# Kernel tuning notes

Measured on AMD Instinct MI355X. Metric: run time of the kernel, lower is better.

The kernel has to match this reference:

```python
import jax, jax.numpy as jnp
import numpy as np

B, S, V, E, H, EMB = 512, 400, 50000, 512, 256, 128


def setup_inputs() -> dict:
    key = jax.random.key(0)
    ks = jax.random.split(key, 20)
    f = lambda i, shape, s=1.0: jax.random.normal(ks[i], shape, jnp.float32) * s
    return dict(
        coverage=jax.random.uniform(ks[0], (B, S), jnp.float32),
        enc_out=f(1, (B, S, E)),
        h0=f(2, (B, H)),
        c0=f(3, (B, H)),
        attn=jax.nn.softmax(f(4, (B, S)), axis=1),
        dec_input=jax.random.randint(ks[5], (B, 1), 0, V),
        enc_inputs=jax.random.randint(ks[6], (B, S), 0, V),
        emb_table=f(7, (V, EMB), 0.02),
        W_ih=f(8, (4 * H, EMB + E), 0.05),
        W_hh=f(9, (4 * H, H), 0.05),
        b_ih=jnp.zeros(4 * H, jnp.float32),
        b_hh=jnp.zeros(4 * H, jnp.float32),
        awh_W=f(10, (H, E), 0.05),
        awh_b=jnp.zeros(H, jnp.float32),
        aws_W=f(11, (H, H), 0.05),
        aws_b=jnp.zeros(H, jnp.float32),
        awc=jax.random.uniform(ks[12], (H,), jnp.float32),
        av=jax.random.uniform(ks[13], (H,), jnp.float32),
        wh=jax.random.uniform(ks[14], (E,), jnp.float32),
        ws=jax.random.uniform(ks[15], (H,), jnp.float32),
        wx=jax.random.uniform(ks[16], (EMB,), jnp.float32),
        v_W=f(17, (V, H), 0.05),
        v_b=jnp.zeros(V, jnp.float32),
    )


def reference(coverage, enc_out, h0, c0, attn, dec_input, enc_inputs,
              emb_table, W_ih, W_hh, b_ih, b_hh,
              awh_W, awh_b, aws_W, aws_b, awc, av,
              wh, ws, wx, v_W, v_b):
    b, s, e = enc_out.shape
    vocab = emb_table.shape[0]

    # context = bmm(attn[B,1,S], enc_out[B,S,E]) -> [B,1,E]
    context = jnp.einsum('bs,bse->be', attn, enc_out)  # [B,E]
    embed = emb_table[dec_input[:, 0]]                 # [B,EMB]
    x = jnp.concatenate([context, embed], axis=1)      # [B,E+EMB]

    # LSTMCell (torch gate order: i, f, g, o)
    gates = x @ W_ih.T + b_ih + h0 @ W_hh.T + b_hh     # [B,4H]
    i, f_, g, o = jnp.split(gates, 4, axis=1)
    c_t = jax.nn.sigmoid(f_) * c0 + jax.nn.sigmoid(i) * jnp.tanh(g)
    h_t = jax.nn.sigmoid(o) * jnp.tanh(c_t)

    p_vocab = jax.nn.softmax(h_t @ v_W.T + v_b, axis=1)  # [B,V]
    p_gen = jax.nn.sigmoid(context @ wh + h_t @ ws + embed @ wx)[:, None]  # [B,1]

    # Bahdanau attention with coverage
    wh_app = jnp.einsum('bse,he->bsh', enc_out, awh_W) + awh_b  # [B,S,H]
    ws_app = (h_t @ aws_W.T + aws_b)[:, None, :]                # [B,1,H]
    wc_app = coverage[:, :, None] * awc                         # [B,S,H]
    energy = jnp.tanh(wh_app + ws_app + wc_app) @ av            # [B,S]
    new_attn = jax.nn.softmax(energy, axis=1)

    coverage_loss = jnp.sum(jnp.minimum(new_attn, coverage))
    new_coverage = coverage + new_attn

    attn_scores = jnp.zeros((b, vocab), p_vocab.dtype).at[jnp.arange(b)[:, None], enc_inputs].set(new_attn)

    output = p_gen * p_vocab + (1.0 - p_gen) * attn_scores
    return output, new_coverage, (h_t, c_t), new_attn, coverage_loss
```

## Files before the change

### kernel.cpp

```cpp
#include <hip/hip_runtime.h>
#include <math.h>

#define Bd   512
#define Sd   400
#define Vd   50000
#define Ed   512
#define Hd   256
#define EMBd 128
#define XHs  896
#define Gd   1024

#define OFF_COV  25600000
#define OFF_H    25804800
#define OFF_C    25935872
#define OFF_ATTN 26066944
#define OFF_LOSS 26271744

#define WS_XH     0
#define WS_GATES  458752
#define WS_WSAPP  983040
#define WS_PGEN   1114112
#define WS_ENERGY 1114624
#define WS_LOSSB  1319424
#define WS_RMAX   1319936
#define WS_RSCALE 1320448
#define WS_HTBF   589824

typedef __attribute__((ext_vector_type(8))) short short8;
typedef __attribute__((ext_vector_type(4))) float f32x4;

__device__ __forceinline__ float sigmoid_f(float x){ return 1.f/(1.f + __expf(-x)); }
__device__ __forceinline__ float tanh_f(float x){ return 1.f - 2.f/(__expf(2.f*x) + 1.f); }

__device__ __forceinline__ void gload_lds16(const void* g, void* l){
  __builtin_amdgcn_global_load_lds((const __attribute__((address_space(1))) void*)g,
                                   (__attribute__((address_space(3))) void*)l, 16, 0, 0);
}

__global__ __launch_bounds__(256) void k_context(
    const float* __restrict__ attn, const float* __restrict__ enc_out,
    const float* __restrict__ h0, const int* __restrict__ dec_input,
    const float* __restrict__ emb_table, float* __restrict__ xh)
{
  int b = blockIdx.x, t = threadIdx.x;
  __shared__ float sa[Sd];
  for (int s = t; s < Sd; s += 256) sa[s] = attn[(size_t)b*Sd + s];
  __syncthreads();
  const float* ep = enc_out + (size_t)b*Sd*Ed;
  float acc0 = 0.f, acc1 = 0.f;
  #pragma unroll 4
  for (int s = 0; s < Sd; ++s){
    float a = sa[s];
    acc0 += a * ep[(size_t)s*Ed + t];
    acc1 += a * ep[(size_t)s*Ed + t + 256];
  }
  float* xrow = xh + (size_t)b*XHs;
  xrow[t]       = acc0;
  xrow[t + 256] = acc1;
  if (t < EMBd){
    int tok = dec_input[b];
    xrow[Ed + t] = emb_table[(size_t)tok*EMBd + t];
  }
  xrow[Ed + EMBd + t] = h0[(size_t)b*Hd + t];
}

__global__ __launch_bounds__(256) void k_gates(
    const float* __restrict__ xh, const float* __restrict__ W_ih,
    const float* __restrict__ W_hh, const float* __restrict__ b_ih,
    const float* __restrict__ b_hh, float* __restrict__ gates)
{
  __shared__ float Al[32*36];
  __shared__ float Wl[64*33];
  int tid = threadIdx.x;
  int col0 = blockIdx.x * 64;
  int row0 = blockIdx.y * 32;
  int cg = tid & 15, rg = tid >> 4;
  float acc[2][4] = {{0,0,0,0},{0,0,0,0}};
  int alr = tid >> 3, alk = (tid & 7) * 4;
  int wlj = tid >> 2, wlk = (tid & 3) * 8;
  for (int kt = 0; kt < 28; ++kt){
    int k0 = kt * 32;
    float4 a4 = *(const float4*)(xh + (size_t)(row0+alr)*XHs + k0 + alk);
    *(float4*)(Al + alr*36 + alk) = a4;
    {
      const float* src;
      if (k0 < Ed + EMBd) src = W_ih + (size_t)(col0+wlj)*(Ed+EMBd) + k0 + wlk;
      else                src = W_hh + (size_t)(col0+wlj)*Hd + (k0 - (Ed+EMBd)) + wlk;
      #pragma unroll
      for (int q = 0; q < 8; ++q) Wl[wlj*33 + wlk + q] = src[q];
    }
    __syncthreads();
    #pragma unroll 4
    for (int k = 0; k < 32; ++k){
      float a0 = Al[(rg*2+0)*36 + k];
      float a1 = Al[(rg*2+1)*36 + k];
      #pragma unroll
      for (int j = 0; j < 4; ++j){
        float w = Wl[(cg + 16*j)*33 + k];
        acc[0][j] += a0 * w;
        acc[1][j] += a1 * w;
      }
    }
    __syncthreads();
  }
  #pragma unroll
  for (int i = 0; i < 2; ++i){
    int row = row0 + rg*2 + i;
    #pragma unroll
    for (int j = 0; j < 4; ++j){
      int col = col0 + cg + 16*j;
      gates[(size_t)row*Gd + col] = acc[i][j] + b_ih[col] + b_hh[col];
    }
  }
}

__global__ __launch_bounds__(256) void k_lstm(
    const float* __restrict__ gates, const float* __restrict__ c0,
    float* __restrict__ dout)
{
  int idx = blockIdx.x*256 + threadIdx.x;
  int b = idx >> 8, h = idx & 255;
  const float* g = gates + (size_t)b*Gd;
  float xi = g[h], xf = g[Hd + h], xg = g[2*Hd + h], xo = g[3*Hd + h];
  float c  = sigmoid_f(xf)*c0[idx] + sigmoid_f(xi)*tanh_f(xg);
  float ht = sigmoid_f(xo)*tanh_f(c);
  dout[OFF_C + idx] = c;
  dout[OFF_H + idx] = ht;
}

__global__ __launch_bounds__(256) void k_wcvt(
    const float* __restrict__ W, short* __restrict__ hi, short* __restrict__ lo,
    const float* __restrict__ ht, short* __restrict__ htb)
{
  int bx = blockIdx.x;
  if (bx < 128){
    int i = bx*256 + threadIdx.x;
    float4 w = ((const float4*)W)[i];
    float xs[4] = {w.x, w.y, w.z, w.w};
    short h4[4], l4[4];
    #pragma unroll
    for (int j = 0; j < 4; ++j){
      unsigned u = __float_as_uint(xs[j]);
      h4[j] = (short)(u >> 16);
      float hf = __uint_as_float(u & 0xffff0000u);
      l4[j] = (short)(__float_as_uint(xs[j] - hf) >> 16);
    }
    ((short4*)hi)[i] = make_short4(h4[0], h4[1], h4[2], h4[3]);
    ((short4*)lo)[i] = make_short4(l4[0], l4[1], l4[2], l4[3]);
  } else {
    int i = (bx - 128)*256 + threadIdx.x;
    float4 w = ((const float4*)ht)[i];
    short h4[4];
    h4[0] = (short)((__float_as_uint(w.x) + 0x8000u) >> 16);
    h4[1] = (short)((__float_as_uint(w.y) + 0x8000u) >> 16);
    h4[2] = (short)((__float_as_uint(w.z) + 0x8000u) >> 16);
    h4[3] = (short)((__float_as_uint(w.w) + 0x8000u) >> 16);
    ((short4*)htb)[i] = make_short4(h4[0], h4[1], h4[2], h4[3]);
  }
}

__global__ __launch_bounds__(256) void k_post(
    const float* __restrict__ ht, const float* __restrict__ aws_W,
    const float* __restrict__ aws_b, const float* __restrict__ xh,
    const float* __restrict__ wh, const float* __restrict__ wsv,
    const float* __restrict__ wx, float* __restrict__ wsapp,
    float* __restrict__ pgen)
{
  int b = blockIdx.x, t = threadIdx.x;
  __shared__ float hrow[Hd];
  __shared__ float red[256];
  float htv = ht[(size_t)b*Hd + t];
  hrow[t] = htv;
  __syncthreads();
  const float4* w4 = (const float4*)(aws_W + (size_t)t*Hd);
  float acc = 0.f;
  #pragma unroll 4
  for (int k4 = 0; k4 < Hd/4; ++k4){
    float4 w = w4[k4];
    int k = k4*4;
    acc += hrow[k]*w.x + hrow[k+1]*w.y + hrow[k+2]*w.z + hrow[k+3]*w.w;
  }
  wsapp[(size_t)b*Hd + t] = acc + aws_b[t];
  const float* x = xh + (size_t)b*XHs;
  float part = x[t]*wh[t] + x[t+256]*wh[t+256];
  part += htv * wsv[t];
  if (t < EMBd) part += x[Ed + t] * wx[t];
  red[t] = part; __syncthreads();
  for (int off = 128; off > 0; off >>= 1){
    if (t < off) red[t] += red[t + off];
    __syncthreads();
  }
  if (t == 0) pgen[b] = sigmoid_f(red[0]);
}

__global__ __launch_bounds__(256) void k_energy_mfma(
    const float* __restrict__ enc_out, const short* __restrict__ Whi,
    const short* __restrict__ Wlo, const float* __restrict__ awh_b,
    const float* __restrict__ wsapp, const float* __restrict__ coverage,
    const float* __restrict__ awc, const float* __restrict__ av,
    float* __restrict__ energy)
{
  __shared__ short Ah[64*32], Alo[64*32];
  __shared__ short Bh[256*32], Blo[256*32];
  int tid = threadIdx.x;
  int wid = tid >> 6, lane = tid & 63;
  int row0 = blockIdx.x * 64;

  f32x4 acc[4][4] = {};

  int ar = tid >> 2, as_ = tid & 3;
  int a_st = ar*32 + (as_ ^ ((ar>>1)&3))*8;
  const float* ag = enc_out + (size_t)(row0 + ar)*Ed + as_*8;

  int b_r[4], b_s[4];
  #pragma unroll
  for (int c = 0; c < 4; ++c){
    int ch = wid*4 + c;
    int r  = ch*16 + (lane>>2);
    b_r[c] = r;
    b_s[c] = (lane&3) ^ ((r>>1)&3);
  }

  int n0 = wid*64;
  int a_rd[4], b_rd[4];
  #pragma unroll
  for (int m = 0; m < 4; ++m){
    int r = m*16 + (lane&15);
    a_rd[m] = r*32 + (((lane>>4) ^ ((r>>1)&3)))*8;
  }
  #pragma unroll
  for (int n = 0; n < 4; ++n){
    int c = n0 + n*16 + (lane&15);
    b_rd[n] = c*32 + (((lane>>4) ^ ((c>>1)&3)))*8;
  }

  for (int kt = 0; kt < Ed/32; ++kt){
    int k0 = kt*32;
    #pragma unroll
    for (int c = 0; c < 4; ++c){
      int ch = wid*4 + c;
      const short* gh = Whi + (size_t)b_r[c]*Ed + k0 + b_s[c]*8;
      const short* gl = Wlo + (size_t)b_r[c]*Ed + k0 + b_s[c]*8;
      gload_lds16(gh, &Bh[ch*512]);
      gload_lds16(gl, &Blo[ch*512]);
    }
    float4 a0 = *(const float4*)(ag + k0);
    float4 a1 = *(const float4*)(ag + k0 + 4);
    float xs[8] = {a0.x,a0.y,a0.z,a0.w,a1.x,a1.y,a1.z,a1.w};
    short8 h8, l8;
    #pragma unroll
    for (int q = 0; q < 8; ++q){
      unsigned u = __float_as_uint(xs[q]);
      h8[q] = (short)(u >> 16);
      float hf = __uint_as_float(u & 0xffff0000u);
      l8[q] = (short)(__float_as_uint(xs[q] - hf) >> 16);
    }
    *(short8*)&Ah[a_st]  = h8;
    *(short8*)&Alo[a_st] = l8;
    __syncthreads();

    short8 ah[4], al[4], bh[4], bl[4];
    #pragma unroll
    for (int m = 0; m < 4; ++m){
      ah[m] = *(const short8*)&Ah[a_rd[m]];
      al[m] = *(const short8*)&Alo[a_rd[m]];
    }
    #pragma unroll
    for (int n = 0; n < 4; ++n){
      bh[n] = *(const short8*)&Bh[b_rd[n]];
      bl[n] = *(const short8*)&Blo[b_rd[n]];
    }
    #pragma unroll
    for (int m = 0; m < 4; ++m){
      #pragma unroll
      for (int n = 0; n < 4; ++n){
        acc[m][n] = __builtin_amdgcn_mfma_f32_16x16x32_bf16(ah[m], bh[n], acc[m][n], 0, 0, 0);
        acc[m][n] = __builtin_amdgcn_mfma_f32_16x16x32_bf16(ah[m], bl[n], acc[m][n], 0, 0, 0);
        acc[m][n] = __builtin_amdgcn_mfma_f32_16x16x32_bf16(al[m], bh[n], acc[m][n], 0, 0, 0);
      }
    }
    __syncthreads();
  }

  float* red = (float*)Bh;
  int b0 = row0 / Sd;
  int b1 = b0 + 1; if (b1 > Bd-1) b1 = Bd-1;
  int split = (b0 + 1) * Sd;
  float avv[4], bbv[4], wcv[4], wv0[4], wv1[4];
  #pragma unroll
  for (int n = 0; n < 4; ++n){
    int h = n0 + n*16 + (lane&15);
    avv[n] = av[h]; bbv[n] = awh_b[h]; wcv[n] = awc[h];
    wv0[n] = wsapp[(size_t)b0*Hd + h];
    wv1[n] = wsapp[(size_t)b1*Hd + h];
  }
  #pragma unroll
  for (int m = 0; m < 4; ++m){
    #pragma unroll
    for (int j = 0; j < 4; ++j){
      int rt = m*16 + ((lane>>4)<<2) + j;
      int grow = row0 + rt;
      bool hib = (grow >= split);
      float cov = coverage[grow];
      float part = 0.f;
      #pragma unroll
      for (int n = 0; n < 4; ++n){
        float x = acc[m][n][j] + bbv[n] + (hib ? wv1[n] : wv0[n]) + cov*wcv[n];
        part += avv[n]*tanh_f(x);
      }
      part += __shfl_xor(part, 1, 16);
      part += __shfl_xor(part, 2, 16);
      part += __shfl_xor(part, 4, 16);
      part += __shfl_xor(part, 8, 16);
      if ((lane & 15) == 0) red[wid*64 + rt] = part;
    }
  }
  __syncthreads();
  if (tid < 64)
    energy[row0 + tid] = red[tid] + red[64 + tid] + red[128 + tid] + red[192 + tid];
}

__global__ __launch_bounds__(256) void k_attn_softmax(
    const float* __restrict__ energy, const float* __restrict__ coverage,
    float* __restrict__ dout, float* __restrict__ loss_b)
{
  int b = blockIdx.x, t = threadIdx.x;
  __shared__ float red[256];
  const float* e = energy + (size_t)b*Sd;
  float e0 = e[t];
  float e1 = (t + 256 < Sd) ? e[t+256] : -1e30f;
  red[t] = fmaxf(e0, e1); __syncthreads();
  for (int off = 128; off > 0; off >>= 1){
    if (t < off) red[t] = fmaxf(red[t], red[t+off]);
    __syncthreads();
  }
  float m = red[0]; __syncthreads();
  float p0 = __expf(e0 - m);
  float p1 = (t + 256 < Sd) ? __expf(e1 - m) : 0.f;
  red[t] = p0 + p1; __syncthreads();
  for (int off = 128; off > 0; off >>= 1){
    if (t < off) red[t] += red[t+off];
    __syncthreads();
  }
  float inv = 1.f / red[0]; __syncthreads();
  float* attn_o = dout + OFF_ATTN + (size_t)b*Sd;
  float* cov_o  = dout + OFF_COV  + (size_t)b*Sd;
  float a0 = p0 * inv;
  float cv0 = coverage[(size_t)b*Sd + t];
  attn_o[t] = a0; cov_o[t] = cv0 + a0;
  float lp = fminf(a0, cv0);
  if (t + 256 < Sd){
    float a1 = p1 * inv;
    float cv1 = coverage[(size_t)b*Sd + t + 256];
    attn_o[t+256] = a1; cov_o[t+256] = cv1 + a1;
    lp += fminf(a1, cv1);
  }
  red[t] = lp; __syncthreads();
  for (int off = 128; off > 0; off >>= 1){
    if (t < off) red[t] += red[t+off];
    __syncthreads();
  }
  if (t == 0) loss_b[b] = red[0];
}

__global__ void k_loss(const float* __restrict__ loss_b, float* __restrict__ dout)
{
  __shared__ float red[256];
  int t = threadIdx.x;
  red[t] = loss_b[t] + loss_b[t + 256];
  __syncthreads();
  for (int off = 128; off > 0; off >>= 1){
    if (t < off) red[t] += red[t+off];
    __syncthreads();
  }
  if (t == 0) dout[OFF_LOSS] = red[0];
}

__global__ __launch_bounds__(256) void k_logits_mfma(
    const short* __restrict__ ht_bf, const float* __restrict__ v_W,
    const float* __restrict__ v_b, float* __restrict__ out)
{
  __shared__ short Abf[128*32];
  __shared__ short Bbf[256*32];
  int tid = threadIdx.x;
  int wid = tid >> 6, lane = tid & 63;
  int col0 = blockIdx.x * 256;
  int row0 = blockIdx.y * 128;
  int wr0 = (wid & 1) * 64, wc0 = (wid >> 1) * 128;

  f32x4 acc[4][8] = {};

  int ac_r[2], ac_s[2];
  #pragma unroll
  for (int c = 0; c < 2; ++c){
    int ch = wid*2 + c;
    int r = ch*16 + (lane >> 2);
    ac_r[c] = r;
    ac_s[c] = (lane & 3) ^ ((r >> 1) & 3);
  }

  int vrow = col0 + tid; if (vrow > Vd - 1) vrow = Vd - 1;
  const float* bg = v_W + (size_t)vrow * Hd;
  int bsw = (tid >> 1) & 3;

  int a_rd[4], b_rd[8];
  #pragma unroll
  for (int m = 0; m < 4; ++m){
    int r = wr0 + m*16 + (lane & 15);
    a_rd[m] = r*32 + (((lane >> 4) ^ ((r >> 1) & 3)))*8;
  }
  #pragma unroll
  for (int n = 0; n < 8; ++n){
    int c = wc0 + n*16 + (lane & 15);
    b_rd[n] = c*32 + (((lane >> 4) ^ ((c >> 1) & 3)))*8;
  }

  for (int kt = 0; kt < Hd/32; ++kt){
    int k0 = kt * 32;
    #pragma unroll
    for (int c = 0; c < 2; ++c){
      const short* src = ht_bf + (size_t)(row0 + ac_r[c])*Hd + k0 + ac_s[c]*8;
      gload_lds16(src, &Abf[(wid*2 + c)*512]);
    }
    unsigned p[16];
    #pragma unroll
    for (int q = 0; q < 8; ++q){
      float4 f = *(const float4*)(bg + k0 + q*4);
      unsigned u0 = __float_as_uint(f.x) + 0x8000u;
      unsigned u1 = __float_as_uint(f.y) + 0x8000u;
      unsigned u2 = __float_as_uint(f.z) + 0x8000u;
      unsigned u3 = __float_as_uint(f.w) + 0x8000u;
      p[q*2]   = (u1 & 0xffff0000u) | (u0 >> 16);
      p[q*2+1] = (u3 & 0xffff0000u) | (u2 >> 16);
    }
    #pragma unroll
    for (int s = 0; s < 4; ++s){
      uint4 w4; w4.x = p[s*4]; w4.y = p[s*4+1]; w4.z = p[s*4+2]; w4.w = p[s*4+3];
      *(uint4*)&Bbf[tid*32 + (s ^ bsw)*8] = w4;
    }
    __syncthreads();
    short8 a[4];
    #pragma unroll
    for (int m = 0; m < 4; ++m) a[m] = *(const short8*)&Abf[a_rd[m]];
    #pragma unroll
    for (int n = 0; n < 8; ++n){
      short8 bfr = *(const short8*)&Bbf[b_rd[n]];
      #pragma unroll
      for (int m = 0; m < 4; ++m)
        acc[m][n] = __builtin_amdgcn_mfma_f32_16x16x32_bf16(a[m], bfr, acc[m][n], 0, 0, 0);
    }
    __syncthreads();
  }

  #pragma unroll
  for (int n = 0; n < 8; ++n){
    int col = col0 + wc0 + n*16 + (lane & 15);
    if (col < Vd){
      float bias = v_b[col];
      #pragma unroll
      for (int m = 0; m < 4; ++m){
        int rbase = row0 + wr0 + m*16 + ((lane >> 4) << 2);
        #pragma unroll
        for (int j = 0; j < 4; ++j)
          out[(size_t)(rbase + j)*Vd + col] = acc[m][n][j] + bias;
      }
    }
  }
}

__global__ __launch_bounds__(256) void k_vocab_stats(
    const float* __restrict__ logits, const float* __restrict__ pgen,
    float* __restrict__ rmax, float* __restrict__ rscale)
{
  int b = blockIdx.x, t = threadIdx.x;
  __shared__ float red[256];
  const float4* row = (const float4*)(logits + (size_t)b*Vd);
  float m = -1e30f;
  for (int i = t; i < Vd/4; i += 256){
    float4 x = row[i];
    m = fmaxf(m, fmaxf(fmaxf(x.x, x.y), fmaxf(x.z, x.w)));
  }
  red[t] = m; __syncthreads();
  for (int off = 128; off > 0; off >>= 1){
    if (t < off) red[t] = fmaxf(red[t], red[t+off]);
    __syncthreads();
  }
  m = red[0]; __syncthreads();
  float s = 0.f;
  for (int i = t; i < Vd/4; i += 256){
    float4 x = row[i];
    s += __expf(x.x-m) + __expf(x.y-m) + __expf(x.z-m) + __expf(x.w-m);
  }
  red[t] = s; __syncthreads();
  for (int off = 128; off > 0; off >>= 1){
    if (t < off) red[t] += red[t+off];
    __syncthreads();
  }
  if (t == 0){ rmax[b] = m; rscale[b] = pgen[b] / red[0]; }
}

__global__ __launch_bounds__(256) void k_vocab_norm(
    float* __restrict__ out, const float* __restrict__ rmax,
    const float* __restrict__ rscale)
{
  long long i4 = (long long)blockIdx.x*256 + threadIdx.x;
  int b = (int)(i4 / (Vd/4));
  float m = rmax[b], sc = rscale[b];
  float4* o = (float4*)out;
  float4 x = o[i4];
  x.x = sc*__expf(x.x - m); x.y = sc*__expf(x.y - m);
  x.z = sc*__expf(x.z - m); x.w = sc*__expf(x.w - m);
  o[i4] = x;
}

__global__ __launch_bounds__(256) void k_scatter(
    const int* __restrict__ enc_inputs, const float* __restrict__ pgen,
    float* __restrict__ dout)
{
  int idx = blockIdx.x*256 + threadIdx.x;
  int b = idx / Sd, s = idx - b*Sd;
  const int* row = enc_inputs + (size_t)b*Sd;
  int v = row[s];
  for (int s2 = s+1; s2 < Sd; ++s2) if (row[s2] == v) return;
  float pg = pgen[b];
  float a = dout[OFF_ATTN + idx];
  float* p = dout + (size_t)b*Vd + v;
  *p = *p + (1.f - pg)*a;
}

extern "C" void kernel_launch(void* const* d_in, const int* in_sizes, int n_in,
                              void* d_out, int out_size, void* d_ws, size_t ws_size,
                              hipStream_t stream)
{
  const float* coverage   = (const float*)d_in[0];
  const float* enc_out    = (const float*)d_in[1];
  const float* h0         = (const float*)d_in[2];
  const float* c0         = (const float*)d_in[3];
  const float* attn       = (const float*)d_in[4];
  const int*   dec_input  = (const int*)  d_in[5];
  const int*   enc_inputs = (const int*)  d_in[6];
  const float* emb_table  = (const float*)d_in[7];
  const float* W_ih       = (const float*)d_in[8];
  const float* W_hh       = (const float*)d_in[9];
  const float* b_ih       = (const float*)d_in[10];
  const float* b_hh       = (const float*)d_in[11];
  const float* awh_W      = (const float*)d_in[12];
  const float* awh_b      = (const float*)d_in[13];
  const float* aws_W      = (const float*)d_in[14];
  const float* aws_b      = (const float*)d_in[15];
  const float* awc        = (const float*)d_in[16];
  const float* av         = (const float*)d_in[17];
  const float* wh         = (const float*)d_in[18];
  const float* wsv        = (const float*)d_in[19];
  const float* wx         = (const float*)d_in[20];
  const float* v_W        = (const float*)d_in[21];
  const float* v_b        = (const float*)d_in[22];
  float* out = (float*)d_out;
  float* ws  = (float*)d_ws;

  float* xh     = ws + WS_XH;
  float* gates  = ws + WS_GATES;
  float* wsapp  = ws + WS_WSAPP;
  float* pgen   = ws + WS_PGEN;
  float* energy = ws + WS_ENERGY;
  float* loss_b = ws + WS_LOSSB;
  float* rmax   = ws + WS_RMAX;
  float* rscale = ws + WS_RSCALE;
  float* ht = out + OFF_H;

  short* Whi   = (short*)gates;
  short* Wlo   = Whi + 256*512;
  short* ht_bf = (short*)(ws + WS_HTBF);

  k_context<<<Bd, 256, 0, stream>>>(attn, enc_out, h0, dec_input, emb_table, xh);
  k_gates<<<dim3(Gd/64, Bd/32), 256, 0, stream>>>(xh, W_ih, W_hh, b_ih, b_hh, gates);
  k_lstm<<<(Bd*Hd)/256, 256, 0, stream>>>(gates, c0, out);
  k_wcvt<<<256, 256, 0, stream>>>(awh_W, Whi, Wlo, ht, ht_bf);
  k_post<<<Bd, 256, 0, stream>>>(ht, aws_W, aws_b, xh, wh, wsv, wx, wsapp, pgen);
  k_energy_mfma<<<(Bd*Sd)/64, 256, 0, stream>>>(enc_out, Whi, Wlo, awh_b, wsapp, coverage, awc, av, energy);
  k_attn_softmax<<<Bd, 256, 0, stream>>>(energy, coverage, out, loss_b);
  k_loss<<<1, 256, 0, stream>>>(loss_b, out);
  k_logits_mfma<<<dim3((Vd + 255)/256, Bd/128), 256, 0, stream>>>(ht_bf, v_W, v_b, out);
  k_vocab_stats<<<Bd, 256, 0, stream>>>(out, pgen, rmax, rscale);
  k_vocab_norm<<<(Bd*Vd/4)/256, 256, 0, stream>>>(out, rmax, rscale);
  k_scatter<<<(Bd*Sd)/256, 256, 0, stream>>>(enc_inputs, pgen, out);
}
```

Before: 1.161 ms.

## Double-buffer energy GEMM, stage logits stores via LDS, vectorize context reduction

The energy MFMA kernel now double-buffers its LDS tiles, so the next K-slice loads from global memory overlap with the MFMAs on the current slice. It also drops one barrier per iteration. The logits kernel stages each 16-row accumulator chunk through shared memory and writes coalesced float4 rows with the bias added, instead of scattered scalar stores. The context kernel switches to float4 loads split over two sequence halves, and the vocab-stats loops get unroll pragmas. The cost is doubled LDS in the energy kernel, which may reduce occupancy, and extra barriers in the logits epilogue.

```diff
diff --git a/kernel.cpp b/kernel.cpp
--- a/kernel.cpp
+++ b/kernel.cpp
@@ -44,19 +44,26 @@
 {
   int b = blockIdx.x, t = threadIdx.x;
   __shared__ float sa[Sd];
+  __shared__ float4 r4[128];
   for (int s = t; s < Sd; s += 256) sa[s] = attn[(size_t)b*Sd + s];
   __syncthreads();
-  const float* ep = enc_out + (size_t)b*Sd*Ed;
-  float acc0 = 0.f, acc1 = 0.f;
+  const float4* ep4 = (const float4*)(enc_out + (size_t)b*Sd*Ed);
+  int cq = t & 127, sp = t >> 7;
+  float4 acc = {0.f, 0.f, 0.f, 0.f};
   #pragma unroll 4
-  for (int s = 0; s < Sd; ++s){
+  for (int s = sp; s < Sd; s += 2){
     float a = sa[s];
-    acc0 += a * ep[(size_t)s*Ed + t];
-    acc1 += a * ep[(size_t)s*Ed + t + 256];
-  }
+    float4 v = ep4[(size_t)s*128 + cq];
+    acc.x += a*v.x; acc.y += a*v.y; acc.z += a*v.z; acc.w += a*v.w;
+  }
+  if (sp) r4[cq] = acc;
+  __syncthreads();
   float* xrow = xh + (size_t)b*XHs;
-  xrow[t]       = acc0;
-  xrow[t + 256] = acc1;
+  if (!sp){
+    float4 o = r4[cq];
+    o.x += acc.x; o.y += acc.y; o.z += acc.z; o.w += acc.w;
+    *(float4*)(xrow + cq*4) = o;
+  }
   if (t < EMBd){
     int tok = dec_input[b];
     xrow[Ed + t] = emb_table[(size_t)tok*EMBd + t];
@@ -200,8 +207,8 @@
     const float* __restrict__ awc, const float* __restrict__ av,
     float* __restrict__ energy)
 {
-  __shared__ short Ah[64*32], Alo[64*32];
-  __shared__ short Bh[256*32], Blo[256*32];
+  __shared__ short Ah[2][64*32], Alo[2][64*32];
+  __shared__ short Bh[2][256*32], Blo[2][256*32];
   int tid = threadIdx.x;
   int wid = tid >> 6, lane = tid & 63;
   int row0 = blockIdx.x * 64;
@@ -234,18 +241,15 @@
     b_rd[n] = c*32 + (((lane>>4) ^ ((c>>1)&3)))*8;
   }
 
-  for (int kt = 0; kt < Ed/32; ++kt){
-    int k0 = kt*32;
-    #pragma unroll
-    for (int c = 0; c < 4; ++c){
-      int ch = wid*4 + c;
-      const short* gh = Whi + (size_t)b_r[c]*Ed + k0 + b_s[c]*8;
-      const short* gl = Wlo + (size_t)b_r[c]*Ed + k0 + b_s[c]*8;
-      gload_lds16(gh, &Bh[ch*512]);
-      gload_lds16(gl, &Blo[ch*512]);
-    }
-    float4 a0 = *(const float4*)(ag + k0);
-    float4 a1 = *(const float4*)(ag + k0 + 4);
+  #pragma unroll
+  for (int c = 0; c < 4; ++c){
+    int ch = wid*4 + c;
+    gload_lds16(Whi + (size_t)b_r[c]*Ed + b_s[c]*8, &Bh[0][ch*512]);
+    gload_lds16(Wlo + (size_t)b_r[c]*Ed + b_s[c]*8, &Blo[0][ch*512]);
+  }
+  {
+    float4 a0 = *(const float4*)(ag);
+    float4 a1 = *(const float4*)(ag + 4);
     float xs[8] = {a0.x,a0.y,a0.z,a0.w,a1.x,a1.y,a1.z,a1.w};
     short8 h8, l8;
     #pragma unroll
@@ -255,20 +259,22 @@
       float hf = __uint_as_float(u & 0xffff0000u);
       l8[q] = (short)(__float_as_uint(xs[q] - hf) >> 16);
     }
-    *(short8*)&Ah[a_st]  = h8;
-    *(short8*)&Alo[a_st] = l8;
-    __syncthreads();
-
+    *(short8*)&Ah[0][a_st]  = h8;
+    *(short8*)&Alo[0][a_st] = l8;
+  }
+  __syncthreads();
+
+  auto compute = [&](int bi){
     short8 ah[4], al[4], bh[4], bl[4];
     #pragma unroll
     for (int m = 0; m < 4; ++m){
-      ah[m] = *(const short8*)&Ah[a_rd[m]];
-      al[m] = *(const short8*)&Alo[a_rd[m]];
+      ah[m] = *(const short8*)&Ah[bi][a_rd[m]];
+      al[m] = *(const short8*)&Alo[bi][a_rd[m]];
     }
     #pragma unroll
     for (int n = 0; n < 4; ++n){
-      bh[n] = *(const short8*)&Bh[b_rd[n]];
-      bl[n] = *(const short8*)&Blo[b_rd[n]];
+      bh[n] = *(const short8*)&Bh[bi][b_rd[n]];
+      bl[n] = *(const short8*)&Blo[bi][b_rd[n]];
     }
     #pragma unroll
     for (int m = 0; m < 4; ++m){
@@ -279,8 +285,36 @@
         acc[m][n] = __builtin_amdgcn_mfma_f32_16x16x32_bf16(al[m], bh[n], acc[m][n], 0, 0, 0);
       }
     }
-    __syncthreads();
-  }
+  };
+
+  for (int kt = 0; kt < 15; ++kt){
+    int cur = kt & 1, nxt = cur ^ 1;
+    int k1 = (kt + 1) * 32;
+    #pragma unroll
+    for (int c = 0; c < 4; ++c){
+      int ch = wid*4 + c;
+      gload_lds16(Whi + (size_t)b_r[c]*Ed + k1 + b_s[c]*8, &Bh[nxt][ch*512]);
+      gload_lds16(Wlo + (size_t)b_r[c]*Ed + k1 + b_s[c]*8, &Blo[nxt][ch*512]);
+    }
+    float4 a0 = *(const float4*)(ag + k1);
+    float4 a1 = *(const float4*)(ag + k1 + 4);
+    compute(cur);
+    {
+      float xs[8] = {a0.x,a0.y,a0.z,a0.w,a1.x,a1.y,a1.z,a1.w};
+      short8 h8, l8;
+      #pragma unroll
+      for (int q = 0; q < 8; ++q){
+        unsigned u = __float_as_uint(xs[q]);
+        h8[q] = (short)(u >> 16);
+        float hf = __uint_as_float(u & 0xffff0000u);
+        l8[q] = (short)(__float_as_uint(xs[q] - hf) >> 16);
+      }
+      *(short8*)&Ah[nxt][a_st]  = h8;
+      *(short8*)&Alo[nxt][a_st] = l8;
+    }
+    __syncthreads();
+  }
+  compute(1);
 
   float* red = (float*)Bh;
   int b0 = row0 / Sd;
@@ -380,8 +414,9 @@
     const short* __restrict__ ht_bf, const float* __restrict__ v_W,
     const float* __restrict__ v_b, float* __restrict__ out)
 {
-  __shared__ short Abf[128*32];
-  __shared__ short Bbf[256*32];
+  __shared__ __align__(16) float smem_f[6144];
+  short* Abf = (short*)smem_f;
+  short* Bbf = Abf + 128*32;
   int tid = threadIdx.x;
   int wid = tid >> 6, lane = tid & 63;
   int col0 = blockIdx.x * 256;
@@ -452,17 +487,36 @@
     __syncthreads();
   }
 
-  #pragma unroll
-  for (int n = 0; n < 8; ++n){
-    int col = col0 + wc0 + n*16 + (lane & 15);
-    if (col < Vd){
-      float bias = v_b[col];
+  float* Cch = smem_f;
+  #pragma unroll
+  for (int ch = 0; ch < 8; ++ch){
+    __syncthreads();
+    int m = ch & 3;
+    if ((wid & 1) == (ch >> 2)){
       #pragma unroll
-      for (int m = 0; m < 4; ++m){
-        int rbase = row0 + wr0 + m*16 + ((lane >> 4) << 2);
+      for (int n = 0; n < 8; ++n){
+        int col = wc0 + n*16 + (lane & 15);
+        int rl = (lane >> 4) << 2;
         #pragma unroll
         for (int j = 0; j < 4; ++j)
-          out[(size_t)(rbase + j)*Vd + col] = acc[m][n][j] + bias;
+          Cch[(rl + j)*260 + col] = acc[m][n][j];
+      }
+    }
+    __syncthreads();
+    int row = tid >> 4;
+    int gr = row0 + ch*16 + row;
+    float* orow = out + (size_t)gr*Vd;
+    #pragma unroll
+    for (int q = 0; q < 4; ++q){
+      int cq = (tid & 15) + 16*q;
+      int col = col0 + cq*4;
+      if (col < Vd){
+        const float* cc = Cch + row*260 + cq*4;
+        float4 vb = *(const float4*)(v_b + col);
+        float4 v;
+        v.x = cc[0] + vb.x; v.y = cc[1] + vb.y;
+        v.z = cc[2] + vb.z; v.w = cc[3] + vb.w;
+        *(float4*)(orow + col) = v;
       }
     }
   }
@@ -476,6 +530,7 @@
   __shared__ float red[256];
   const float4* row = (const float4*)(logits + (size_t)b*Vd);
   float m = -1e30f;
+  #pragma unroll 4
   for (int i = t; i < Vd/4; i += 256){
     float4 x = row[i];
     m = fmaxf(m, fmaxf(fmaxf(x.x, x.y), fmaxf(x.z, x.w)));
@@ -487,6 +542,7 @@
   }
   m = red[0]; __syncthreads();
   float s = 0.f;
+  #pragma unroll 4
   for (int i = t; i < Vd/4; i += 256){
     float4 x = row[i];
     s += __expf(x.x-m) + __expf(x.y-m) + __expf(x.z-m) + __expf(x.w-m);
```

Result: slower. 1.198 ms (+3.2%).
